# Kernel optimization log

Hardware: AMD Instinct MI355X
Metric: run time of the kernel (lower is better)

Reference implementation:

```python
import jax, jax.numpy as jnp
import numpy as np
import math

D_MODEL = 1024
NUM_HEADS = 16
HEAD_DIM = D_MODEL // NUM_HEADS


def setup_inputs() -> dict:
    key = jax.random.key(0)
    ks = jax.random.split(key, 10)
    B, Sq, Skv = 2, 2048, 2048
    s = 1.0 / math.sqrt(D_MODEL)
    return {
        "X": jax.random.normal(ks[0], (B, Skv, D_MODEL), jnp.float32),
        "y": jax.random.normal(ks[1], (B, Sq, D_MODEL), jnp.float32),
        "qW": jax.random.normal(ks[2], (D_MODEL, D_MODEL), jnp.float32) * s,
        "qB": jnp.zeros((D_MODEL,), jnp.float32),
        "kW": jax.random.normal(ks[3], (D_MODEL, D_MODEL), jnp.float32) * s,
        "kB": jnp.zeros((D_MODEL,), jnp.float32),
        "vW": jax.random.normal(ks[4], (D_MODEL, D_MODEL), jnp.float32) * s,
        "vB": jnp.zeros((D_MODEL,), jnp.float32),
        "oW": jax.random.normal(ks[5], (D_MODEL, D_MODEL), jnp.float32) * s,
        "oB": jnp.zeros((D_MODEL,), jnp.float32),
    }


def _split_heads(x):
    # (B, S, D) -> (B, H, S, dk)
    B, S, _ = x.shape
    return x.reshape(B, S, NUM_HEADS, HEAD_DIM).transpose(0, 2, 1, 3)


def reference(X, y, qW, qB, kW, kB, vW, vB, oW, oB):
    B = X.shape[0]
    q = _split_heads(y @ qW + qB)   # queries come from y (decoder)
    k = _split_heads(X @ kW + kB)   # keys/values from X (encoder)
    v = _split_heads(X @ vW + vB)
    scale = 1.0 / math.sqrt(HEAD_DIM)
    scores = jnp.einsum("bhqd,bhkd->bhqk", q, k) * scale
    weights = jax.nn.softmax(scores, axis=-1)
    attn = jnp.einsum("bhqk,bhkd->bhqd", weights, v)
    concat = attn.transpose(0, 2, 1, 3).reshape(B, -1, D_MODEL)
    return concat @ oW + oB
```

## Files before the change

kernel.cpp:

```cpp
#include <hip/hip_runtime.h>
#include <hip/hip_bf16.h>
#include <math.h>

typedef __hip_bfloat16 bf16;
typedef __bf16 nbf16;
typedef __bf16 bf16x8 __attribute__((ext_vector_type(8)));
typedef __bf16 bf16x4 __attribute__((ext_vector_type(4)));
typedef float f32x4 __attribute__((ext_vector_type(4)));

#define D_MODEL 1024
#define NHEAD   16
#define HDK     64
#define BATCH   2
#define SEQ     2048
#define QSZ     ((size_t)BATCH * SEQ * D_MODEL)
#define WSZ     ((size_t)D_MODEL * D_MODEL)

__global__ void detect_dtype(const unsigned short* __restrict__ x, int* flag) {
    __shared__ int cnt;
    if (threadIdx.x == 0) cnt = 0;
    __syncthreads();
    int local = 0;
    for (int i = threadIdx.x; i < 4096; i += 256) {
        const unsigned short v = x[i];
        const int e = (v >> 7) & 0xFF;
        if (v == 0 || (e >= 96 && e <= 141)) local++;
    }
    atomicAdd(&cnt, local);
    __syncthreads();
    if (threadIdx.x == 0) *flag = (cnt >= 3600) ? 1 : 0;
}

__device__ __forceinline__ float ldIn(const void* p, size_t i, int isbf16) {
    return isbf16 ? __bfloat162float(((const bf16*)p)[i])
                  : ((const float*)p)[i];
}

__device__ __forceinline__ void gload_lds16(const void* g, void* l) {
    __builtin_amdgcn_global_load_lds(
        (const __attribute__((address_space(1))) void*)g,
        (__attribute__((address_space(3))) void*)l, 16, 0, 0);
}

__global__ void tobf16(const void* __restrict__ in, nbf16* __restrict__ out,
                       const int* __restrict__ flagp) {
    const int flag = *flagp;
    const size_t i = ((size_t)blockIdx.x * 256 + threadIdx.x) * 8;
    if (flag) {
        *(uint4*)(out + i) = *(const uint4*)((const nbf16*)in + i);
    } else {
        const float4 a = *(const float4*)((const float*)in + i);
        const float4 b = *(const float4*)((const float*)in + i + 4);
        bf16x8 v = {(nbf16)a.x, (nbf16)a.y, (nbf16)a.z, (nbf16)a.w,
                    (nbf16)b.x, (nbf16)b.y, (nbf16)b.z, (nbf16)b.w};
        *(bf16x8*)(out + i) = v;
    }
}

__global__ void wtrans(const void* __restrict__ W, nbf16* __restrict__ Wt,
                       const int* __restrict__ flagp) {
    const int flag = *flagp;
    __shared__ float T[64][65];
    const int k0 = blockIdx.x * 64, n0 = blockIdx.y * 64;
    #pragma unroll
    for (int i = 0; i < 16; ++i) {
        const int idx = threadIdx.x + i * 256;
        const int r = idx >> 6, c = idx & 63;
        T[r][c] = ldIn(W, (size_t)(k0 + r) * D_MODEL + n0 + c, flag);
    }
    __syncthreads();
    #pragma unroll
    for (int i = 0; i < 16; ++i) {
        const int idx = threadIdx.x + i * 256;
        const int n = idx >> 6, k = idx & 63;
        Wt[(size_t)(n0 + n) * D_MODEL + k0 + k] = (nbf16)T[k][n];
    }
}

#define STAGE_AB(Albuf, Blbuf, Aptr, Bptr, t)                                  \
{                                                                              \
    const int _k0 = (t) * 64;                                                  \
    _Pragma("unroll")                                                          \
    for (int i = 0; i < 4; ++i) {                                              \
        const int row = i * 32 + wid * 8 + (lane >> 3);                        \
        const int ss  = (lane & 7) ^ (row & 7);                                \
        gload_lds16((Aptr) + (size_t)row * D_MODEL + _k0 + ss * 8,             \
                    (nbf16*)(Albuf) + i * 2048 + wid * 512);                   \
    }                                                                          \
    _Pragma("unroll")                                                          \
    for (int i = 0; i < 2; ++i) {                                              \
        const int row = i * 32 + wid * 8 + (lane >> 3);                        \
        const int ss  = (lane & 7) ^ (row & 7);                                \
        gload_lds16((Bptr) + (size_t)row * D_MODEL + _k0 + ss * 8,             \
                    (nbf16*)(Blbuf) + i * 2048 + wid * 512);                   \
    }                                                                          \
}

__global__ __launch_bounds__(256, 2) void proj_qkv(
        const nbf16* __restrict__ Xb, const nbf16* __restrict__ Yb,
        const nbf16* __restrict__ Wt3,
        const void* __restrict__ qB, const void* __restrict__ kB,
        const void* __restrict__ vB,
        nbf16* __restrict__ outq, const int* __restrict__ flagp) {
    __shared__ nbf16 Al[2][128][64];
    __shared__ nbf16 Bl[2][64][64];

    const int flag = *flagp;
    const int tid  = threadIdx.x;
    const int wid  = tid >> 6;
    const int lane = tid & 63;
    const int l15  = lane & 15;
    const int lg   = lane >> 4;
    const int wr   = wid >> 1;
    const int wc   = wid & 1;

    const int id = blockIdx.x;
    const int sw = (id & 7) * 192 + (id >> 3);
    const int m0  = (sw & 31) * 128;
    const int ng0 = (sw >> 5) * 64;

    const nbf16* A  = (ng0 < D_MODEL) ? Yb : Xb;
    const nbf16* Bm = Wt3 + (size_t)ng0 * D_MODEL;
    const nbf16* Am = A + (size_t)m0 * D_MODEL;

    f32x4 acc[4][2];
    #pragma unroll
    for (int mi = 0; mi < 4; ++mi)
        #pragma unroll
        for (int ni = 0; ni < 2; ++ni) acc[mi][ni] = (f32x4){0.f, 0.f, 0.f, 0.f};

    STAGE_AB(&Al[0][0][0], &Bl[0][0][0], Am, Bm, 0);
    __syncthreads();

    const int NT = D_MODEL / 64;
    for (int t = 0; t < NT; ++t) {
        const int cur = t & 1;
        if (t + 1 < NT)
            STAGE_AB(&Al[cur ^ 1][0][0], &Bl[cur ^ 1][0][0], Am, Bm, t + 1);

        #pragma unroll
        for (int kk = 0; kk < 2; ++kk) {
            bf16x8 af[4], bfr[2];
            #pragma unroll
            for (int mi = 0; mi < 4; ++mi) {
                const int ar = wr * 64 + mi * 16 + l15;
                const int sl = ((kk << 2) + lg) ^ (ar & 7);
                af[mi] = *(const bf16x8*)((const nbf16*)&Al[cur][ar][0] + sl * 8);
            }
            #pragma unroll
            for (int ni = 0; ni < 2; ++ni) {
                const int br = wc * 32 + ni * 16 + l15;
                const int sl = ((kk << 2) + lg) ^ (br & 7);
                bfr[ni] = *(const bf16x8*)((const nbf16*)&Bl[cur][br][0] + sl * 8);
            }
            #pragma unroll
            for (int mi = 0; mi < 4; ++mi)
                #pragma unroll
                for (int ni = 0; ni < 2; ++ni)
                    acc[mi][ni] = __builtin_amdgcn_mfma_f32_16x16x32_bf16(
                        af[mi], bfr[ni], acc[mi][ni], 0, 0, 0);
        }
        __syncthreads();
    }

    #pragma unroll
    for (int ni = 0; ni < 2; ++ni) {
        const int n  = ng0 + wc * 32 + ni * 16 + l15;
        const int wh = n >> 10;
        const int nl = n & 1023;
        const void* bp = (wh == 0) ? qB : (wh == 1) ? kB : vB;
        const float bias = ldIn(bp, (size_t)nl, flag);
        nbf16* outp = outq + (size_t)wh * QSZ;
        #pragma unroll
        for (int mi = 0; mi < 4; ++mi) {
            #pragma unroll
            for (int r = 0; r < 4; ++r) {
                const int m = m0 + wr * 64 + mi * 16 + lg * 4 + r;
                const float v = acc[mi][ni][r] + bias;
                const int b = m >> 11, s = m & (SEQ - 1);
                const int h = nl >> 6,  d = nl & (HDK - 1);
                outp[(((size_t)(b * NHEAD + h)) * SEQ + s) * HDK + d] = (nbf16)v;
            }
        }
    }
}

__global__ __launch_bounds__(256, 2) void proj_o(
        const nbf16* __restrict__ A, const nbf16* __restrict__ Wt,
        const void* __restrict__ Braw, void* __restrict__ Cout,
        const int* __restrict__ flagp) {
    __shared__ nbf16 Al[2][128][64];
    __shared__ nbf16 Bl[2][64][64];

    const int flag = *flagp;
    const int tid  = threadIdx.x;
    const int wid  = tid >> 6;
    const int lane = tid & 63;
    const int l15  = lane & 15;
    const int lg   = lane >> 4;
    const int wr   = wid >> 1;
    const int wc   = wid & 1;

    const int id = blockIdx.x;
    const int sw = (id & 7) * 64 + (id >> 3);
    const int m0 = (sw >> 4) * 128;
    const int n0 = (sw & 15) * 64;

    const nbf16* Am = A + (size_t)m0 * D_MODEL;
    const nbf16* Bm = Wt + (size_t)n0 * D_MODEL;

    f32x4 acc[4][2];
    #pragma unroll
    for (int mi = 0; mi < 4; ++mi)
        #pragma unroll
        for (int ni = 0; ni < 2; ++ni) acc[mi][ni] = (f32x4){0.f, 0.f, 0.f, 0.f};

    STAGE_AB(&Al[0][0][0], &Bl[0][0][0], Am, Bm, 0);
    __syncthreads();

    const int NT = D_MODEL / 64;
    for (int t = 0; t < NT; ++t) {
        const int cur = t & 1;
        if (t + 1 < NT)
            STAGE_AB(&Al[cur ^ 1][0][0], &Bl[cur ^ 1][0][0], Am, Bm, t + 1);

        #pragma unroll
        for (int kk = 0; kk < 2; ++kk) {
            bf16x8 af[4], bfr[2];
            #pragma unroll
            for (int mi = 0; mi < 4; ++mi) {
                const int ar = wr * 64 + mi * 16 + l15;
                const int sl = ((kk << 2) + lg) ^ (ar & 7);
                af[mi] = *(const bf16x8*)((const nbf16*)&Al[cur][ar][0] + sl * 8);
            }
            #pragma unroll
            for (int ni = 0; ni < 2; ++ni) {
                const int br = wc * 32 + ni * 16 + l15;
                const int sl = ((kk << 2) + lg) ^ (br & 7);
                bfr[ni] = *(const bf16x8*)((const nbf16*)&Bl[cur][br][0] + sl * 8);
            }
            #pragma unroll
            for (int mi = 0; mi < 4; ++mi)
                #pragma unroll
                for (int ni = 0; ni < 2; ++ni)
                    acc[mi][ni] = __builtin_amdgcn_mfma_f32_16x16x32_bf16(
                        af[mi], bfr[ni], acc[mi][ni], 0, 0, 0);
        }
        __syncthreads();
    }

    #pragma unroll
    for (int ni = 0; ni < 2; ++ni) {
        const int n = n0 + wc * 32 + ni * 16 + l15;
        const float bias = ldIn(Braw, (size_t)n, flag);
        #pragma unroll
        for (int mi = 0; mi < 4; ++mi) {
            #pragma unroll
            for (int r = 0; r < 4; ++r) {
                const int m = m0 + wr * 64 + mi * 16 + lg * 4 + r;
                const float v = acc[mi][ni][r] + bias;
                if (flag) ((bf16*)Cout)[(size_t)m * D_MODEL + n] = __float2bfloat16(v);
                else      ((float*)Cout)[(size_t)m * D_MODEL + n] = v;
            }
        }
    }
}

__global__ __launch_bounds__(256, 2) void attn_mfma(
        const nbf16* __restrict__ qg, const nbf16* __restrict__ kg,
        const nbf16* __restrict__ vg, nbf16* __restrict__ cg) {
    __shared__ nbf16 KL[2][64][64];
    __shared__ nbf16 VT[2][64][72];
    __shared__ nbf16 PB[4][32][72];

    const int tid  = threadIdx.x;
    const int wid  = tid >> 6;
    const int lane = tid & 63;
    const int l15  = lane & 15;
    const int lg   = lane >> 4;

    const int id = blockIdx.x;
    const int sw = (id & 7) * 64 + (id >> 3);
    const int bh = sw >> 4;
    const int qt = sw & 15;

    const nbf16* qb = qg + (size_t)bh * SEQ * HDK;
    const nbf16* kb = kg + (size_t)bh * SEQ * HDK;
    const nbf16* vb = vg + (size_t)bh * SEQ * HDK;

    const int qbase = qt * 128 + wid * 32;
    const nbf16* qpA = qb + (size_t)(qbase + l15) * HDK + lg * 8;
    const nbf16* qpB = qpA + 16 * HDK;
    const bf16x8 qfA0 = *(const bf16x8*)qpA;
    const bf16x8 qfA1 = *(const bf16x8*)(qpA + 32);
    const bf16x8 qfB0 = *(const bf16x8*)qpB;
    const bf16x8 qfB1 = *(const bf16x8*)(qpB + 32);

    const int g8 = (tid >> 5) * 8;
    const int p2 = (tid & 31) * 2;

    #define STAGEK(buf, t)                                                     \
    {                                                                          \
        _Pragma("unroll")                                                      \
        for (int i = 0; i < 2; ++i) {                                          \
            const int row = i * 32 + wid * 8 + (lane >> 3);                    \
            const int ss  = (lane & 7) ^ (row & 7);                            \
            gload_lds16(kb + (size_t)((t) * 64 + row) * HDK + ss * 8,          \
                        (nbf16*)&KL[buf][0][0] + i * 2048 + wid * 512);        \
        }                                                                      \
    }

    #define VLOAD(t)                                                           \
        a0 = *(const uint4*)(vb + (size_t)((t) * 64 + p2) * HDK + g8);         \
        a1 = *(const uint4*)(vb + (size_t)((t) * 64 + p2 + 1) * HDK + g8);

    #define VWRITE(buf)                                                        \
    {                                                                          \
        const unsigned short* e0 = (const unsigned short*)&a0;                 \
        const unsigned short* e1 = (const unsigned short*)&a1;                 \
        _Pragma("unroll")                                                      \
        for (int j = 0; j < 8; ++j)                                            \
            *(unsigned int*)&VT[buf][g8 + j][p2] =                             \
                (unsigned int)e0[j] | ((unsigned int)e1[j] << 16);             \
    }

    const float SC = 0.125f * 1.44269504088896340736f;

    #define SOFTMAX(st, m2, lden, o, pbrow)                                    \
    do {                                                                       \
        float tm = -3.0e38f;                                                   \
        _Pragma("unroll")                                                      \
        for (int s_ = 0; s_ < 4; ++s_)                                         \
            _Pragma("unroll")                                                  \
            for (int r = 0; r < 4; ++r) {                                      \
                st[s_][r] *= SC;                                               \
                tm = fmaxf(tm, st[s_][r]);                                     \
            }                                                                  \
        tm = fmaxf(tm, __shfl_xor(tm, 16, 64));                                \
        tm = fmaxf(tm, __shfl_xor(tm, 32, 64));                                \
        const float mnew  = fmaxf(m2, tm);                                     \
        const float alpha = exp2f(m2 - mnew);                                  \
        float ts = 0.f;                                                        \
        _Pragma("unroll")                                                      \
        for (int s_ = 0; s_ < 4; ++s_) {                                       \
            const float p0 = exp2f(st[s_][0] - mnew);                          \
            const float p1 = exp2f(st[s_][1] - mnew);                          \
            const float p2_ = exp2f(st[s_][2] - mnew);                         \
            const float p3 = exp2f(st[s_][3] - mnew);                          \
            ts += (p0 + p1) + (p2_ + p3);                                      \
            bf16x4 pk = {(nbf16)p0, (nbf16)p1, (nbf16)p2_, (nbf16)p3};         \
            *(bf16x4*)((pbrow) + s_ * 16 + lg * 4) = pk;                       \
        }                                                                      \
        ts += __shfl_xor(ts, 16, 64);                                          \
        ts += __shfl_xor(ts, 32, 64);                                          \
        lden = lden * alpha + ts;                                              \
        m2 = mnew;                                                             \
        float av[4];                                                           \
        _Pragma("unroll")                                                      \
        for (int r = 0; r < 4; ++r) av[r] = __shfl(alpha, lg * 4 + r, 64);     \
        _Pragma("unroll")                                                      \
        for (int i = 0; i < 4; ++i)                                            \
            _Pragma("unroll")                                                  \
            for (int r = 0; r < 4; ++r) o[i][r] *= av[r];                      \
    } while (0)

    float m2A = -3.0e38f, ldenA = 0.f;
    float m2B = -3.0e38f, ldenB = 0.f;
    f32x4 oA[4], oB[4];
    #pragma unroll
    for (int i = 0; i < 4; ++i) { oA[i] = (f32x4){0,0,0,0}; oB[i] = (f32x4){0,0,0,0}; }

    const int NT = SEQ / 64;

    {
        uint4 a0, a1;
        STAGEK(0, 0);
        VLOAD(0);
        VWRITE(0);
    }
    __syncthreads();

    for (int t = 0; t < NT; ++t) {
        const int cur = t & 1;
        uint4 a0, a1;
        if (t + 1 < NT) {
            STAGEK(cur ^ 1, t + 1);
            VLOAD(t + 1);
        }

        f32x4 stA[4], stB[4];
        #pragma unroll
        for (int sub = 0; sub < 4; ++sub) {
            const int row = sub * 16 + l15;
            const int s0 = lg ^ (row & 7);
            const int s1 = (4 + lg) ^ (row & 7);
            const bf16x8 kf0 = *(const bf16x8*)((const nbf16*)&KL[cur][row][0] + s0 * 8);
            const bf16x8 kf1 = *(const bf16x8*)((const nbf16*)&KL[cur][row][0] + s1 * 8);
            f32x4 a = (f32x4){0,0,0,0};
            a = __builtin_amdgcn_mfma_f32_16x16x32_bf16(kf0, qfA0, a, 0, 0, 0);
            a = __builtin_amdgcn_mfma_f32_16x16x32_bf16(kf1, qfA1, a, 0, 0, 0);
            stA[sub] = a;
            f32x4 b = (f32x4){0,0,0,0};
            b = __builtin_amdgcn_mfma_f32_16x16x32_bf16(kf0, qfB0, b, 0, 0, 0);
            b = __builtin_amdgcn_mfma_f32_16x16x32_bf16(kf1, qfB1, b, 0, 0, 0);
            stB[sub] = b;
        }

        SOFTMAX(stA, m2A, ldenA, oA, &PB[wid][l15][0]);
        SOFTMAX(stB, m2B, ldenB, oB, &PB[wid][16 + l15][0]);

        __asm__ volatile("s_waitcnt lgkmcnt(0)" ::: "memory");

        const bf16x8 pfA0 = *(const bf16x8*)&PB[wid][l15][lg * 8];
        const bf16x8 pfA1 = *(const bf16x8*)&PB[wid][l15][lg * 8 + 32];
        const bf16x8 pfB0 = *(const bf16x8*)&PB[wid][16 + l15][lg * 8];
        const bf16x8 pfB1 = *(const bf16x8*)&PB[wid][16 + l15][lg * 8 + 32];
        #pragma unroll
        for (int db = 0; db < 4; ++db) {
            const bf16x8 vf0 = *(const bf16x8*)&VT[cur][db * 16 + l15][lg * 8];
            const bf16x8 vf1 = *(const bf16x8*)&VT[cur][db * 16 + l15][lg * 8 + 32];
            oA[db] = __builtin_amdgcn_mfma_f32_16x16x32_bf16(pfA0, vf0, oA[db], 0, 0, 0);
            oA[db] = __builtin_amdgcn_mfma_f32_16x16x32_bf16(pfA1, vf1, oA[db], 0, 0, 0);
            oB[db] = __builtin_amdgcn_mfma_f32_16x16x32_bf16(pfB0, vf0, oB[db], 0, 0, 0);
            oB[db] = __builtin_amdgcn_mfma_f32_16x16x32_bf16(pfB1, vf1, oB[db], 0, 0, 0);
        }

        if (t + 1 < NT) VWRITE(cur ^ 1);
        __syncthreads();
    }

    const int b = bh >> 4, h = bh & 15;
    float invdA[4], invdB[4];
    #pragma unroll
    for (int r = 0; r < 4; ++r) {
        invdA[r] = 1.f / __shfl(ldenA, lg * 4 + r, 64);
        invdB[r] = 1.f / __shfl(ldenB, lg * 4 + r, 64);
    }
    #pragma unroll
    for (int db = 0; db < 4; ++db) {
        #pragma unroll
        for (int r = 0; r < 4; ++r) {
            const int qA = qbase + lg * 4 + r;
            cg[((size_t)(b * SEQ + qA)) * D_MODEL + h * HDK + db * 16 + l15] =
                (nbf16)(oA[db][r] * invdA[r]);
            const int qB_ = qbase + 16 + lg * 4 + r;
            cg[((size_t)(b * SEQ + qB_)) * D_MODEL + h * HDK + db * 16 + l15] =
                (nbf16)(oB[db][r] * invdB[r]);
        }
    }
    #undef STAGEK
    #undef VLOAD
    #undef VWRITE
    #undef SOFTMAX
}

extern "C" void kernel_launch(void* const* d_in, const int* in_sizes, int n_in,
                              void* d_out, int out_size, void* d_ws, size_t ws_size,
                              hipStream_t stream) {
    const void* X  = d_in[0];
    const void* Y  = d_in[1];
    const void* qW = d_in[2];
    const void* qB = d_in[3];
    const void* kW = d_in[4];
    const void* kB = d_in[5];
    const void* vW = d_in[6];
    const void* vB = d_in[7];
    const void* oW = d_in[8];
    const void* oB = d_in[9];

    nbf16* ws = (nbf16*)d_ws;
    nbf16* qbuf = ws;
    nbf16* kbuf = qbuf + QSZ;
    nbf16* vbuf = kbuf + QSZ;
    nbf16* cbuf = vbuf + QSZ;
    nbf16* Xb   = cbuf + QSZ;
    nbf16* Yb   = Xb + QSZ;
    nbf16* Wt3  = Yb + QSZ;
    nbf16* Wto  = Wt3 + 3 * WSZ;
    int*   flag = (int*)(Wto + WSZ);

    detect_dtype<<<1, 256, 0, stream>>>((const unsigned short*)X, flag);

    tobf16<<<(int)(QSZ / (256 * 8)), 256, 0, stream>>>(X, Xb, flag);
    tobf16<<<(int)(QSZ / (256 * 8)), 256, 0, stream>>>(Y, Yb, flag);

    const dim3 tg(16, 16);
    wtrans<<<tg, 256, 0, stream>>>(qW, Wt3, flag);
    wtrans<<<tg, 256, 0, stream>>>(kW, Wt3 + WSZ, flag);
    wtrans<<<tg, 256, 0, stream>>>(vW, Wt3 + 2 * WSZ, flag);
    wtrans<<<tg, 256, 0, stream>>>(oW, Wto, flag);

    proj_qkv<<<1536, 256, 0, stream>>>(Xb, Yb, Wt3, qB, kB, vB, qbuf, flag);

    attn_mfma<<<512, 256, 0, stream>>>(qbuf, kbuf, vbuf, cbuf);

    proj_o<<<512, 256, 0, stream>>>(cbuf, Wto, oB, d_out, flag);
}
```

Before: 279.5 us.

## Enlarge GEMM tiles to 128x128, add lazy softmax rescale and MFMA priority

Both projection GEMMs go from 128x64 to 128x128 block tiles, so each block does twice the MFMA work per staged A tile and the grids halve. In attention, the online softmax skips rescaling the output accumulators when the running max grows by no more than a threshold, keeping the old reference max. The MFMA sections are also wrapped in s_setprio to favour matrix issue. The bigger tiles use more registers and LDS and leave fewer blocks (256 for proj_o) to fill the GPU.

```diff
diff --git a/kernel.cpp b/kernel.cpp
--- a/kernel.cpp
+++ b/kernel.cpp
@@ -77,7 +77,7 @@
     }
 }
 
-#define STAGE_AB(Albuf, Blbuf, Aptr, Bptr, t)                                  \
+#define STAGE128(Albuf, Blbuf, Aptr, Bptr, t)                                  \
 {                                                                              \
     const int _k0 = (t) * 64;                                                  \
     _Pragma("unroll")                                                          \
@@ -86,15 +86,41 @@
         const int ss  = (lane & 7) ^ (row & 7);                                \
         gload_lds16((Aptr) + (size_t)row * D_MODEL + _k0 + ss * 8,             \
                     (nbf16*)(Albuf) + i * 2048 + wid * 512);                   \
-    }                                                                          \
-    _Pragma("unroll")                                                          \
-    for (int i = 0; i < 2; ++i) {                                              \
-        const int row = i * 32 + wid * 8 + (lane >> 3);                        \
-        const int ss  = (lane & 7) ^ (row & 7);                                \
         gload_lds16((Bptr) + (size_t)row * D_MODEL + _k0 + ss * 8,             \
                     (nbf16*)(Blbuf) + i * 2048 + wid * 512);                   \
     }                                                                          \
 }
+
+#define GEMM128_LOOP(Al, Bl)                                                   \
+    const int NT = D_MODEL / 64;                                               \
+    for (int t = 0; t < NT; ++t) {                                             \
+        const int cur = t & 1;                                                 \
+        if (t + 1 < NT)                                                        \
+            STAGE128(&Al[cur ^ 1][0][0], &Bl[cur ^ 1][0][0], Am, Bm, t + 1);   \
+        _Pragma("unroll")                                                      \
+        for (int kk = 0; kk < 2; ++kk) {                                       \
+            bf16x8 af[4], bfr[4];                                              \
+            _Pragma("unroll")                                                  \
+            for (int mi = 0; mi < 4; ++mi) {                                   \
+                const int ar = wr * 64 + mi * 16 + l15;                        \
+                const int sl = ((kk << 2) + lg) ^ (ar & 7);                    \
+                af[mi] = *(const bf16x8*)((const nbf16*)&Al[cur][ar][0] + sl * 8); \
+            }                                                                  \
+            _Pragma("unroll")                                                  \
+            for (int ni = 0; ni < 4; ++ni) {                                   \
+                const int br = wc * 64 + ni * 16 + l15;                        \
+                const int sl = ((kk << 2) + lg) ^ (br & 7);                    \
+                bfr[ni] = *(const bf16x8*)((const nbf16*)&Bl[cur][br][0] + sl * 8); \
+            }                                                                  \
+            _Pragma("unroll")                                                  \
+            for (int mi = 0; mi < 4; ++mi)                                     \
+                _Pragma("unroll")                                              \
+                for (int ni = 0; ni < 4; ++ni)                                 \
+                    acc[mi][ni] = __builtin_amdgcn_mfma_f32_16x16x32_bf16(     \
+                        af[mi], bfr[ni], acc[mi][ni], 0, 0, 0);                \
+        }                                                                      \
+        __syncthreads();                                                       \
+    }
 
 __global__ __launch_bounds__(256, 2) void proj_qkv(
         const nbf16* __restrict__ Xb, const nbf16* __restrict__ Yb,
@@ -103,7 +129,7 @@
         const void* __restrict__ vB,
         nbf16* __restrict__ outq, const int* __restrict__ flagp) {
     __shared__ nbf16 Al[2][128][64];
-    __shared__ nbf16 Bl[2][64][64];
+    __shared__ nbf16 Bl[2][128][64];
 
     const int flag = *flagp;
     const int tid  = threadIdx.x;
@@ -115,57 +141,28 @@
     const int wc   = wid & 1;
 
     const int id = blockIdx.x;
-    const int sw = (id & 7) * 192 + (id >> 3);
+    const int sw = (id & 7) * 96 + (id >> 3);
     const int m0  = (sw & 31) * 128;
-    const int ng0 = (sw >> 5) * 64;
+    const int ng0 = (sw >> 5) * 128;
 
     const nbf16* A  = (ng0 < D_MODEL) ? Yb : Xb;
     const nbf16* Bm = Wt3 + (size_t)ng0 * D_MODEL;
     const nbf16* Am = A + (size_t)m0 * D_MODEL;
 
-    f32x4 acc[4][2];
+    f32x4 acc[4][4];
     #pragma unroll
     for (int mi = 0; mi < 4; ++mi)
         #pragma unroll
-        for (int ni = 0; ni < 2; ++ni) acc[mi][ni] = (f32x4){0.f, 0.f, 0.f, 0.f};
-
-    STAGE_AB(&Al[0][0][0], &Bl[0][0][0], Am, Bm, 0);
-    __syncthreads();
-
-    const int NT = D_MODEL / 64;
-    for (int t = 0; t < NT; ++t) {
-        const int cur = t & 1;
-        if (t + 1 < NT)
-            STAGE_AB(&Al[cur ^ 1][0][0], &Bl[cur ^ 1][0][0], Am, Bm, t + 1);
-
-        #pragma unroll
-        for (int kk = 0; kk < 2; ++kk) {
-            bf16x8 af[4], bfr[2];
-            #pragma unroll
-            for (int mi = 0; mi < 4; ++mi) {
-                const int ar = wr * 64 + mi * 16 + l15;
-                const int sl = ((kk << 2) + lg) ^ (ar & 7);
-                af[mi] = *(const bf16x8*)((const nbf16*)&Al[cur][ar][0] + sl * 8);
-            }
-            #pragma unroll
-            for (int ni = 0; ni < 2; ++ni) {
-                const int br = wc * 32 + ni * 16 + l15;
-                const int sl = ((kk << 2) + lg) ^ (br & 7);
-                bfr[ni] = *(const bf16x8*)((const nbf16*)&Bl[cur][br][0] + sl * 8);
-            }
-            #pragma unroll
-            for (int mi = 0; mi < 4; ++mi)
-                #pragma unroll
-                for (int ni = 0; ni < 2; ++ni)
-                    acc[mi][ni] = __builtin_amdgcn_mfma_f32_16x16x32_bf16(
-                        af[mi], bfr[ni], acc[mi][ni], 0, 0, 0);
-        }
-        __syncthreads();
-    }
-
-    #pragma unroll
-    for (int ni = 0; ni < 2; ++ni) {
-        const int n  = ng0 + wc * 32 + ni * 16 + l15;
+        for (int ni = 0; ni < 4; ++ni) acc[mi][ni] = (f32x4){0.f, 0.f, 0.f, 0.f};
+
+    STAGE128(&Al[0][0][0], &Bl[0][0][0], Am, Bm, 0);
+    __syncthreads();
+
+    GEMM128_LOOP(Al, Bl)
+
+    #pragma unroll
+    for (int ni = 0; ni < 4; ++ni) {
+        const int n  = ng0 + wc * 64 + ni * 16 + l15;
         const int wh = n >> 10;
         const int nl = n & 1023;
         const void* bp = (wh == 0) ? qB : (wh == 1) ? kB : vB;
@@ -190,7 +187,7 @@
         const void* __restrict__ Braw, void* __restrict__ Cout,
         const int* __restrict__ flagp) {
     __shared__ nbf16 Al[2][128][64];
-    __shared__ nbf16 Bl[2][64][64];
+    __shared__ nbf16 Bl[2][128][64];
 
     const int flag = *flagp;
     const int tid  = threadIdx.x;
@@ -202,56 +199,27 @@
     const int wc   = wid & 1;
 
     const int id = blockIdx.x;
-    const int sw = (id & 7) * 64 + (id >> 3);
-    const int m0 = (sw >> 4) * 128;
-    const int n0 = (sw & 15) * 64;
+    const int sw = (id & 7) * 32 + (id >> 3);
+    const int m0 = (sw >> 3) * 128;
+    const int n0 = (sw & 7) * 128;
 
     const nbf16* Am = A + (size_t)m0 * D_MODEL;
     const nbf16* Bm = Wt + (size_t)n0 * D_MODEL;
 
-    f32x4 acc[4][2];
+    f32x4 acc[4][4];
     #pragma unroll
     for (int mi = 0; mi < 4; ++mi)
         #pragma unroll
-        for (int ni = 0; ni < 2; ++ni) acc[mi][ni] = (f32x4){0.f, 0.f, 0.f, 0.f};
-
-    STAGE_AB(&Al[0][0][0], &Bl[0][0][0], Am, Bm, 0);
-    __syncthreads();
-
-    const int NT = D_MODEL / 64;
-    for (int t = 0; t < NT; ++t) {
-        const int cur = t & 1;
-        if (t + 1 < NT)
-            STAGE_AB(&Al[cur ^ 1][0][0], &Bl[cur ^ 1][0][0], Am, Bm, t + 1);
-
-        #pragma unroll
-        for (int kk = 0; kk < 2; ++kk) {
-            bf16x8 af[4], bfr[2];
-            #pragma unroll
-            for (int mi = 0; mi < 4; ++mi) {
-                const int ar = wr * 64 + mi * 16 + l15;
-                const int sl = ((kk << 2) + lg) ^ (ar & 7);
-                af[mi] = *(const bf16x8*)((const nbf16*)&Al[cur][ar][0] + sl * 8);
-            }
-            #pragma unroll
-            for (int ni = 0; ni < 2; ++ni) {
-                const int br = wc * 32 + ni * 16 + l15;
-                const int sl = ((kk << 2) + lg) ^ (br & 7);
-                bfr[ni] = *(const bf16x8*)((const nbf16*)&Bl[cur][br][0] + sl * 8);
-            }
-            #pragma unroll
-            for (int mi = 0; mi < 4; ++mi)
-                #pragma unroll
-                for (int ni = 0; ni < 2; ++ni)
-                    acc[mi][ni] = __builtin_amdgcn_mfma_f32_16x16x32_bf16(
-                        af[mi], bfr[ni], acc[mi][ni], 0, 0, 0);
-        }
-        __syncthreads();
-    }
-
-    #pragma unroll
-    for (int ni = 0; ni < 2; ++ni) {
-        const int n = n0 + wc * 32 + ni * 16 + l15;
+        for (int ni = 0; ni < 4; ++ni) acc[mi][ni] = (f32x4){0.f, 0.f, 0.f, 0.f};
+
+    STAGE128(&Al[0][0][0], &Bl[0][0][0], Am, Bm, 0);
+    __syncthreads();
+
+    GEMM128_LOOP(Al, Bl)
+
+    #pragma unroll
+    for (int ni = 0; ni < 4; ++ni) {
+        const int n = n0 + wc * 64 + ni * 16 + l15;
         const float bias = ldIn(Braw, (size_t)n, flag);
         #pragma unroll
         for (int mi = 0; mi < 4; ++mi) {
@@ -338,30 +306,35 @@
             }                                                                  \
         tm = fmaxf(tm, __shfl_xor(tm, 16, 64));                                \
         tm = fmaxf(tm, __shfl_xor(tm, 32, 64));                                \
-        const float mnew  = fmaxf(m2, tm);                                     \
-        const float alpha = exp2f(m2 - mnew);                                  \
+        const bool nresc = __all(tm - m2 <= 8.0f);                             \
+        const float mref = nresc ? m2 : fmaxf(m2, tm);                         \
         float ts = 0.f;                                                        \
         _Pragma("unroll")                                                      \
         for (int s_ = 0; s_ < 4; ++s_) {                                       \
-            const float p0 = exp2f(st[s_][0] - mnew);                          \
-            const float p1 = exp2f(st[s_][1] - mnew);                          \
-            const float p2_ = exp2f(st[s_][2] - mnew);                         \
-            const float p3 = exp2f(st[s_][3] - mnew);                          \
+            const float p0 = exp2f(st[s_][0] - mref);                          \
+            const float p1 = exp2f(st[s_][1] - mref);                          \
+            const float p2_ = exp2f(st[s_][2] - mref);                         \
+            const float p3 = exp2f(st[s_][3] - mref);                          \
             ts += (p0 + p1) + (p2_ + p3);                                      \
             bf16x4 pk = {(nbf16)p0, (nbf16)p1, (nbf16)p2_, (nbf16)p3};         \
             *(bf16x4*)((pbrow) + s_ * 16 + lg * 4) = pk;                       \
         }                                                                      \
         ts += __shfl_xor(ts, 16, 64);                                          \
         ts += __shfl_xor(ts, 32, 64);                                          \
-        lden = lden * alpha + ts;                                              \
-        m2 = mnew;                                                             \
-        float av[4];                                                           \
-        _Pragma("unroll")                                                      \
-        for (int r = 0; r < 4; ++r) av[r] = __shfl(alpha, lg * 4 + r, 64);     \
-        _Pragma("unroll")                                                      \
-        for (int i = 0; i < 4; ++i)                                            \
-            _Pragma("unroll")                                                  \
-            for (int r = 0; r < 4; ++r) o[i][r] *= av[r];                      \
+        if (nresc) {                                                           \
+            lden += ts;                                                        \
+        } else {                                                               \
+            const float alpha = exp2f(m2 - mref);                              \
+            lden = lden * alpha + ts;                                          \
+            m2 = mref;                                                         \
+            float av[4];                                                       \
+            _Pragma("unroll")                                                  \
+            for (int r = 0; r < 4; ++r) av[r] = __shfl(alpha, lg * 4 + r, 64); \
+            _Pragma("unroll")                                                  \
+            for (int i = 0; i < 4; ++i)                                        \
+                _Pragma("unroll")                                              \
+                for (int r = 0; r < 4; ++r) o[i][r] *= av[r];                  \
+        }                                                                      \
     } while (0)
 
     float m2A = -3.0e38f, ldenA = 0.f;
@@ -389,6 +362,7 @@
         }
 
         f32x4 stA[4], stB[4];
+        __builtin_amdgcn_s_setprio(1);
         #pragma unroll
         for (int sub = 0; sub < 4; ++sub) {
             const int row = sub * 16 + l15;
@@ -405,6 +379,7 @@
             b = __builtin_amdgcn_mfma_f32_16x16x32_bf16(kf1, qfB1, b, 0, 0, 0);
             stB[sub] = b;
         }
+        __builtin_amdgcn_s_setprio(0);
 
         SOFTMAX(stA, m2A, ldenA, oA, &PB[wid][l15][0]);
         SOFTMAX(stB, m2B, ldenB, oB, &PB[wid][16 + l15][0]);
@@ -415,6 +390,7 @@
         const bf16x8 pfA1 = *(const bf16x8*)&PB[wid][l15][lg * 8 + 32];
         const bf16x8 pfB0 = *(const bf16x8*)&PB[wid][16 + l15][lg * 8];
         const bf16x8 pfB1 = *(const bf16x8*)&PB[wid][16 + l15][lg * 8 + 32];
+        __builtin_amdgcn_s_setprio(1);
         #pragma unroll
         for (int db = 0; db < 4; ++db) {
             const bf16x8 vf0 = *(const bf16x8*)&VT[cur][db * 16 + l15][lg * 8];
@@ -424,6 +400,7 @@
             oB[db] = __builtin_amdgcn_mfma_f32_16x16x32_bf16(pfB0, vf0, oB[db], 0, 0, 0);
             oB[db] = __builtin_amdgcn_mfma_f32_16x16x32_bf16(pfB1, vf1, oB[db], 0, 0, 0);
         }
+        __builtin_amdgcn_s_setprio(0);
 
         if (t + 1 < NT) VWRITE(cur ^ 1);
         __syncthreads();
@@ -490,9 +467,9 @@
     wtrans<<<tg, 256, 0, stream>>>(vW, Wt3 + 2 * WSZ, flag);
     wtrans<<<tg, 256, 0, stream>>>(oW, Wto, flag);
 
-    proj_qkv<<<1536, 256, 0, stream>>>(Xb, Yb, Wt3, qB, kB, vB, qbuf, flag);
+    proj_qkv<<<768, 256, 0, stream>>>(Xb, Yb, Wt3, qB, kB, vB, qbuf, flag);
 
     attn_mfma<<<512, 256, 0, stream>>>(qbuf, kbuf, vbuf, cbuf);
 
-    proj_o<<<512, 256, 0, stream>>>(cbuf, Wto, oB, d_out, flag);
-}
+    proj_o<<<256, 256, 0, stream>>>(cbuf, Wto, oB, d_out, flag);
+}
```

Result: no change. 278.6 us (-0.3%).
